# Optimization experiments

Hardware: AMD Instinct MI355X
Metric: run time of the kernel (lower is better)

Reference implementation:

```python
import jax, jax.numpy as jnp
import numpy as np

B, L, H, DH, DM, DFF, V, NL, NP, NT = 4, 2048, 12, 64, 768, 3072, 30522, 12, 2048, 2
LN_EPS = 1e-5       # fast_transformers default LayerNorm eps
EMB_LN_EPS = 1e-12  # BERT embeddings LayerNorm eps
ATT_EPS = 1e-6      # linear attention normalizer eps


def layer_norm(x, w, b, eps):
    m = jnp.mean(x, axis=-1, keepdims=True)
    v = jnp.mean((x - m) ** 2, axis=-1, keepdims=True)
    return (x - m) * jax.lax.rsqrt(v + eps) * w + b


def setup_inputs() -> dict:
    key = jax.random.key(0)
    ks = jax.random.split(key, 24)
    s = 0.02
    d = {
        "input_ids": jax.random.randint(ks[0], (B, L), 0, V),
        "attention_mask": jnp.ones((B, L), jnp.float32),
        "token_type_ids": jnp.zeros((B, L), jnp.int64),
        "word_emb": jax.random.normal(ks[1], (V, DM), jnp.float32) * s,
        "pos_emb": jax.random.normal(ks[2], (NP, DM), jnp.float32) * s,
        "type_emb": jax.random.normal(ks[3], (NT, DM), jnp.float32) * s,
        "emb_ln_w": jnp.ones((DM,), jnp.float32),
        "emb_ln_b": jnp.zeros((DM,), jnp.float32),
        "Wq": jax.random.normal(ks[4], (NL, DM, DM), jnp.float32) * s,
        "bq": jnp.zeros((NL, DM), jnp.float32),
        "Wk": jax.random.normal(ks[5], (NL, DM, DM), jnp.float32) * s,
        "bk": jnp.zeros((NL, DM), jnp.float32),
        "Wv": jax.random.normal(ks[6], (NL, DM, DM), jnp.float32) * s,
        "bv": jnp.zeros((NL, DM), jnp.float32),
        "Wo": jax.random.normal(ks[7], (NL, DM, DM), jnp.float32) * s,
        "bo": jnp.zeros((NL, DM), jnp.float32),
        "ln1_w": jnp.ones((NL, DM), jnp.float32),
        "ln1_b": jnp.zeros((NL, DM), jnp.float32),
        "W1": jax.random.normal(ks[8], (NL, DFF, DM), jnp.float32) * s,
        "b1": jnp.zeros((NL, DFF), jnp.float32),
        "W2": jax.random.normal(ks[9], (NL, DM, DFF), jnp.float32) * s,
        "b2": jnp.zeros((NL, DM), jnp.float32),
        "ln2_w": jnp.ones((NL, DM), jnp.float32),
        "ln2_b": jnp.zeros((NL, DM), jnp.float32),
    }
    return d


def _encoder(x, mask, Wq, bq, Wk, bk, Wv, bv, Wo, bo, ln1_w, ln1_b, W1, b1, W2, b2, ln2_w, ln2_b):
    b, l = x.shape[:2]
    for i in range(NL):
        # linear attention (fast_transformers): phi = elu + 1
        q = (x @ Wq[i].T + bq[i]).reshape(b, l, H, DH)
        k = (x @ Wk[i].T + bk[i]).reshape(b, l, H, DH)
        v = (x @ Wv[i].T + bv[i]).reshape(b, l, H, DH)
        Q = jax.nn.elu(q) + 1.0
        K = (jax.nn.elu(k) + 1.0) * mask[:, :, None, None]  # zero padded keys
        KV = jnp.einsum('nshd,nshm->nhmd', K, v)            # [b,H,DH(m=val),DH(d=key)]
        Z = 1.0 / (jnp.einsum('nlhd,nhd->nlh', Q, K.sum(axis=1)) + ATT_EPS)
        a = jnp.einsum('nlhd,nhmd,nlh->nlhm', Q, KV, Z).reshape(b, l, DM)
        a = a @ Wo[i].T + bo[i]
        x = layer_norm(x + a, ln1_w[i], ln1_b[i], LN_EPS)
        y = jax.nn.gelu(x @ W1[i].T + b1[i], approximate=False)
        y = y @ W2[i].T + b2[i]
        x = layer_norm(x + y, ln2_w[i], ln2_b[i], LN_EPS)
    return x


def reference(input_ids, attention_mask, token_type_ids, word_emb, pos_emb, type_emb,
              emb_ln_w, emb_ln_b, Wq, bq, Wk, bk, Wv, bv, Wo, bo,
              ln1_w, ln1_b, W1, b1, W2, b2, ln2_w, ln2_b):
    b, l = input_ids.shape
    e = word_emb[input_ids] + pos_emb[:l][None, :, :] + type_emb[token_type_ids]
    x = layer_norm(e, emb_ln_w, emb_ln_b, EMB_LN_EPS)
    return _encoder(x, attention_mask, Wq, bq, Wk, bk, Wv, bv, Wo, bo,
                    ln1_w, ln1_b, W1, b1, W2, b2, ln2_w, ln2_b)
```

## Files before the change

### kernel.cpp

```cpp
#include <hip/hip_runtime.h>
#include <math.h>

#define B_   4
#define L_   2048
#define H_   12
#define DH_  64
#define DM_  768
#define DFF_ 3072
#define NL_  12
#define M_   (B_*L_)
#define NCH_ 32
#define QLD_ 2304
#define LN_EPS_  1e-5f
#define EMB_EPS_ 1e-12f
#define ATT_EPS_ 1e-6f

typedef unsigned short u16;
typedef __bf16 bf16x8 __attribute__((ext_vector_type(8)));
typedef float  f32x4  __attribute__((ext_vector_type(4)));

__device__ __forceinline__ u16 f2b(float f) {
  unsigned u = __builtin_bit_cast(unsigned, f);
  u += 0x7fffu + ((u >> 16) & 1u);
  return (u16)(u >> 16);
}
__device__ __forceinline__ float b2f(u16 s) {
  return __builtin_bit_cast(float, (unsigned)((unsigned)s << 16));
}
__device__ __forceinline__ float wredsum(float v) {
  #pragma unroll
  for (int o = 32; o > 0; o >>= 1) v += __shfl_xor(v, o, 64);
  return v;
}
__device__ __forceinline__ void gld16(const void* g, void* l) {
  __builtin_amdgcn_global_load_lds(
      (const __attribute__((address_space(1))) void*)g,
      (__attribute__((address_space(3))) void*)l, 16, 0, 0);
}

__global__ __launch_bounds__(256) void cvt_bf16(const float* __restrict__ in,
                                                u16* __restrict__ out, int n4) {
  int i = blockIdx.x * 256 + threadIdx.x;
  if (i >= n4) return;
  float4 f = ((const float4*)in)[i];
  ushort4 o;
  o.x = f2b(f.x); o.y = f2b(f.y); o.z = f2b(f.z); o.w = f2b(f.w);
  ((ushort4*)out)[i] = o;
}

__global__ __launch_bounds__(256) void cvt_bf16_qkv(const float* __restrict__ in,
                                                    u16* __restrict__ out, int ro) {
  int i = blockIdx.x * 256 + threadIdx.x;
  if (i >= NL_*DM_*DM_/4) return;
  int row = i / 192;
  int c4  = (i % 192) * 4;
  int l = row / DM_, r = row % DM_;
  float4 f = ((const float4*)in)[i];
  ushort4 o;
  o.x = f2b(f.x); o.y = f2b(f.y); o.z = f2b(f.z); o.w = f2b(f.w);
  *(ushort4*)(out + ((size_t)l*QLD_ + ro + r)*DM_ + c4) = o;
}

__global__ __launch_bounds__(256) void fuse_bias(const float* __restrict__ bq,
    const float* __restrict__ bk, const float* __restrict__ bv, float* __restrict__ out) {
  int i = blockIdx.x * 256 + threadIdx.x;
  if (i >= NL_*QLD_) return;
  int l = i / QLD_, r = i % QLD_;
  float v = r < DM_ ? bq[l*DM_ + r] : r < 2*DM_ ? bk[l*DM_ + r - DM_] : bv[l*DM_ + r - 2*DM_];
  out[i] = v;
}

__global__ __launch_bounds__(256) void embed_ln(
    const int* __restrict__ ids, const int* __restrict__ tts,
    const float* __restrict__ we, const float* __restrict__ pe,
    const float* __restrict__ te, const float* __restrict__ lw,
    const float* __restrict__ lb, float* __restrict__ x32, u16* __restrict__ xb)
{
  int row  = blockIdx.x * 4 + (threadIdx.x >> 6);
  int lane = threadIdx.x & 63;
  int l  = row & (L_ - 1);
  int id = ids[row];
  int tt = tts[row];
  const float* wr = we + (size_t)id * DM_;
  const float* pr = pe + (size_t)l  * DM_;
  const float* tr = te + (size_t)tt * DM_;
  float v[12]; float s = 0.f;
  #pragma unroll
  for (int j = 0; j < 12; j++) { int c = j*64 + lane; v[j] = wr[c] + pr[c] + tr[c]; s += v[j]; }
  s = wredsum(s);
  float m = s * (1.f/768.f);
  float q = 0.f;
  #pragma unroll
  for (int j = 0; j < 12; j++) { float d = v[j] - m; q += d*d; }
  q = wredsum(q);
  float rs = rsqrtf(q * (1.f/768.f) + EMB_EPS_);
  float* xo = x32 + (size_t)row * DM_;
  u16*   bo = xb  + (size_t)row * DM_;
  #pragma unroll
  for (int j = 0; j < 12; j++) {
    int c = j*64 + lane;
    float o = (v[j] - m) * rs * lw[c] + lb[c];
    xo[c] = o; bo[c] = f2b(o);
  }
}

__global__ __launch_bounds__(256) void ln_res(
    float* __restrict__ x32, const float* __restrict__ t32,
    const float* __restrict__ lw, const float* __restrict__ lb,
    u16* __restrict__ xb, float eps)
{
  int row  = blockIdx.x * 4 + (threadIdx.x >> 6);
  int lane = threadIdx.x & 63;
  float* xr = x32 + (size_t)row * DM_;
  const float* tr = t32 + (size_t)row * DM_;
  float v[12]; float s = 0.f;
  #pragma unroll
  for (int j = 0; j < 12; j++) { int c = j*64 + lane; v[j] = xr[c] + tr[c]; s += v[j]; }
  s = wredsum(s);
  float m = s * (1.f/768.f);
  float q = 0.f;
  #pragma unroll
  for (int j = 0; j < 12; j++) { float d = v[j] - m; q += d*d; }
  q = wredsum(q);
  float rs = rsqrtf(q * (1.f/768.f) + eps);
  u16* bo = xb + (size_t)row * DM_;
  #pragma unroll
  for (int j = 0; j < 12; j++) {
    int c = j*64 + lane;
    float o = (v[j] - m) * rs * lw[c] + lb[c];
    xr[c] = o; bo[c] = f2b(o);
  }
}

template<int EPI>
__global__ __launch_bounds__(256)
void gemm_gl(const u16* __restrict__ A, const u16* __restrict__ Bw,
             const float* __restrict__ bias,
             u16* __restrict__ Co, float* __restrict__ Cf,
             int M, int N, int K, int ldc)
{
  __shared__ alignas(16) u16 sA[128*32];
  __shared__ alignas(16) u16 sB[128*32];
  const int tid  = threadIdx.x;
  const int lane = tid & 63;
  const int w    = tid >> 6;
  const int wr = w >> 1, wc = w & 1;
  const int row0 = blockIdx.x * 128;
  const int col0 = blockIdx.y * 128;
  const int grow = tid >> 2;
  const int gcol = (tid & 3) * 8;
  const int lr = lane & 15;
  const int lk = (lane >> 4) * 8;

  const u16* Ap = A  + (size_t)(row0 + grow) * K + gcol;
  const u16* Bp = Bw + (size_t)(col0 + grow) * K + gcol;
  u16* sAw0 = sA + w*512;
  u16* sAw1 = sA + 2048 + w*512;
  u16* sBw0 = sB + w*512;
  u16* sBw1 = sB + 2048 + w*512;

  f32x4 acc[4][4];
  #pragma unroll
  for (int i = 0; i < 4; i++)
    #pragma unroll
    for (int j = 0; j < 4; j++) acc[i][j] = (f32x4){0.f,0.f,0.f,0.f};

  for (int kt = 0; kt < K; kt += 32) {
    gld16(Ap + kt,                  sAw0);
    gld16(Ap + kt + (size_t)64*K,   sAw1);
    gld16(Bp + kt,                  sBw0);
    gld16(Bp + kt + (size_t)64*K,   sBw1);
    __syncthreads();
    bf16x8 af[4], bv[4];
    #pragma unroll
    for (int m = 0; m < 4; m++) af[m] = *(const bf16x8*)(sA + (wr*64 + m*16 + lr)*32 + lk);
    #pragma unroll
    for (int n = 0; n < 4; n++) bv[n] = *(const bf16x8*)(sB + (wc*64 + n*16 + lr)*32 + lk);
    #pragma unroll
    for (int m = 0; m < 4; m++)
      #pragma unroll
      for (int n = 0; n < 4; n++)
        acc[m][n] = __builtin_amdgcn_mfma_f32_16x16x32_bf16(af[m], bv[n], acc[m][n], 0, 0, 0);
    __syncthreads();
  }

  #pragma unroll
  for (int m = 0; m < 4; m++) {
    const int row_b = row0 + wr*64 + m*16 + (lane >> 4) * 4;
    #pragma unroll
    for (int n = 0; n < 4; n++) {
      const int col = col0 + wc*64 + n*16 + lr;
      const float bvb = bias[col];
      #pragma unroll
      for (int r = 0; r < 4; r++) {
        float v = acc[m][n][r] + bvb;
        if constexpr (EPI == 4) { if (col < 2*DM_) v = v > 0.f ? v + 1.f : expf(v); }
        if constexpr (EPI == 2) v = 0.5f * v * (1.f + erff(v * 0.70710678118654752f));
        const size_t off = (size_t)(row_b + r) * ldc + col;
        if constexpr (EPI == 3) Cf[off] = v;
        else                    Co[off] = f2b(v);
      }
    }
  }
}

__global__ __launch_bounds__(256)
void gemm_n64(const u16* __restrict__ A, const u16* __restrict__ Bw,
              const float* __restrict__ bias, float* __restrict__ Cf,
              int M, int N, int K, int ldc)
{
  __shared__ alignas(16) u16 sA[128*64];
  __shared__ alignas(16) u16 sB[64*64];
  const int tid  = threadIdx.x;
  const int lane = tid & 63;
  const int w    = tid >> 6;
  const int row0 = blockIdx.x * 128;
  const int col0 = blockIdx.y * 64;
  const int lr = lane & 15;
  const int g  = lane >> 4;
  const int srow = lane >> 3;
  const int acol = (((lane & 7) ^ srow) * 8);

  f32x4 acc[2][4];
  #pragma unroll
  for (int i = 0; i < 2; i++)
    #pragma unroll
    for (int j = 0; j < 4; j++) acc[i][j] = (f32x4){0.f,0.f,0.f,0.f};

  const u16* ApA = A  + (size_t)(row0)*K;
  const u16* BpB = Bw + (size_t)(col0)*K;

  for (int kt = 0; kt < K; kt += 64) {
    #pragma unroll
    for (int j = 0; j < 4; j++)
      gld16(ApA + (size_t)(w*32 + j*8 + srow)*K + kt + acol, sA + (w*32 + j*8)*64);
    #pragma unroll
    for (int j = 0; j < 2; j++)
      gld16(BpB + (size_t)(w*16 + j*8 + srow)*K + kt + acol, sB + (w*16 + j*8)*64);
    __syncthreads();
    #pragma unroll
    for (int kk = 0; kk < 2; kk++) {
      bf16x8 af[2], bv[4];
      #pragma unroll
      for (int m = 0; m < 2; m++) {
        const int R = w*32 + m*16 + lr;
        const int gg = (kk*4 + g) ^ (lr & 7);
        af[m] = *(const bf16x8*)(sA + R*64 + gg*8);
      }
      #pragma unroll
      for (int n = 0; n < 4; n++) {
        const int R = n*16 + lr;
        const int gg = (kk*4 + g) ^ (lr & 7);
        bv[n] = *(const bf16x8*)(sB + R*64 + gg*8);
      }
      #pragma unroll
      for (int m = 0; m < 2; m++)
        #pragma unroll
        for (int n = 0; n < 4; n++)
          acc[m][n] = __builtin_amdgcn_mfma_f32_16x16x32_bf16(af[m], bv[n], acc[m][n], 0, 0, 0);
    }
    __syncthreads();
  }

  #pragma unroll
  for (int m = 0; m < 2; m++) {
    const int row_b = row0 + w*32 + m*16 + (lane >> 4) * 4;
    #pragma unroll
    for (int n = 0; n < 4; n++) {
      const int col = col0 + n*16 + lr;
      const float bvb = bias[col];
      #pragma unroll
      for (int r = 0; r < 4; r++)
        Cf[(size_t)(row_b + r) * ldc + col] = acc[m][n][r] + bvb;
    }
  }
}

__global__ __launch_bounds__(256) void kv_part(
    const u16* __restrict__ qkv, const float* __restrict__ mask,
    float* __restrict__ kvp, float* __restrict__ ksp)
{
  __shared__ float sK[64*64];
  __shared__ float sV[64*64];
  const int bh = blockIdx.x;
  const int b = bh / H_, h = bh % H_;
  const int s0 = blockIdx.y * 64;
  const int t = threadIdx.x;
  const u16* kb = qkv + DM_;
  const u16* vb = qkv + 2*DM_;
  #pragma unroll
  for (int r = 0; r < 2; r++) {
    int idx = r*256 + t;
    int sr = idx >> 3;
    int c  = (idx & 7) * 8;
    int sg = s0 + sr;
    size_t base = ((size_t)(b*L_ + sg)) * QLD_ + h*DH_ + c;
    uint4 kk = *(const uint4*)(kb + base);
    uint4 vv = *(const uint4*)(vb + base);
    float mk = mask[b*L_ + sg];
    const u16* kp = (const u16*)&kk;
    const u16* vp = (const u16*)&vv;
    #pragma unroll
    for (int j = 0; j < 8; j++) {
      sK[sr*64 + c + j] = b2f(kp[j]) * mk;
      sV[sr*64 + c + j] = b2f(vp[j]);
    }
  }
  __syncthreads();
  const int m0 = (t >> 4) * 4;
  const int d0 = (t & 15) * 4;
  float acc[4][4] = {{0.f}};
  float ks[4] = {0.f, 0.f, 0.f, 0.f};
  for (int s = 0; s < 64; s++) {
    float4 vm = *(const float4*)(sV + s*64 + m0);
    float4 kk = *(const float4*)(sK + s*64 + d0);
    float vmv[4] = {vm.x, vm.y, vm.z, vm.w};
    float kkv[4] = {kk.x, kk.y, kk.z, kk.w};
    #pragma unroll
    for (int i = 0; i < 4; i++)
      #pragma unroll
      for (int j = 0; j < 4; j++) acc[i][j] += vmv[i] * kkv[j];
    if (t < 16) { ks[0] += kkv[0]; ks[1] += kkv[1]; ks[2] += kkv[2]; ks[3] += kkv[3]; }
  }
  float* o = kvp + ((size_t)bh*NCH_ + blockIdx.y) * 4096;
  #pragma unroll
  for (int i = 0; i < 4; i++) {
    float4 wv = {acc[i][0], acc[i][1], acc[i][2], acc[i][3]};
    *(float4*)(o + (m0 + i)*64 + d0) = wv;
  }
  if (t < 16) {
    float* ko = ksp + ((size_t)bh*NCH_ + blockIdx.y) * 64;
    #pragma unroll
    for (int j = 0; j < 4; j++) ko[d0 + j] = ks[j];
  }
}

__global__ __launch_bounds__(256) void kv_reduce(
    const float* __restrict__ kvp, const float* __restrict__ ksp,
    float* __restrict__ kv, float* __restrict__ ksum)
{
  const int bh = blockIdx.x;
  const int i = blockIdx.y * 256 + threadIdx.x;
  float s = 0.f;
  #pragma unroll 8
  for (int c = 0; c < NCH_; c++) s += kvp[((size_t)bh*NCH_ + c)*4096 + i];
  kv[(size_t)bh*4096 + i] = s;
  if (blockIdx.y == 0 && threadIdx.x < 64) {
    float q = 0.f;
    #pragma unroll 8
    for (int c = 0; c < NCH_; c++) q += ksp[((size_t)bh*NCH_ + c)*64 + threadIdx.x];
    ksum[bh*64 + threadIdx.x] = q;
  }
}

__global__ __launch_bounds__(256) void attn_av(
    const u16* __restrict__ qkv, const float* __restrict__ kv,
    const float* __restrict__ ksum, u16* __restrict__ ab)
{
  __shared__ alignas(16) u16 sQ[128*72];
  __shared__ alignas(16) u16 sKV[64*72];
  __shared__ float sKs[64];
  __shared__ float sZ[128];
  const int bh = blockIdx.x;
  const int b = bh / H_, h = bh % H_;
  const int l0 = blockIdx.y * 128;
  const int t = threadIdx.x;
  const int lane = t & 63;
  const int w = t >> 6;
  for (int i = t; i < 4096; i += 256)
    sKV[(i >> 6)*72 + (i & 63)] = f2b(kv[(size_t)bh*4096 + i]);
  if (t < 64) sKs[t] = ksum[bh*64 + t];
  #pragma unroll
  for (int r = 0; r < 4; r++) {
    int idx = r*256 + t;
    int s = idx >> 3;
    int c = (idx & 7) * 8;
    *(uint4*)(sQ + s*72 + c) =
        *(const uint4*)(qkv + ((size_t)(b*L_ + l0 + s)) * QLD_ + h*DH_ + c);
  }
  __syncthreads();
  {
    int row = t >> 1, half = t & 1;
    float zd = 0.f;
    #pragma unroll
    for (int ch = 0; ch < 4; ch++) {
      bf16x8 qv = *(const bf16x8*)(sQ + row*72 + half*32 + ch*8);
      #pragma unroll
      for (int j = 0; j < 8; j++) zd += (float)qv[j] * sKs[half*32 + ch*8 + j];
    }
    zd += __shfl_xor(zd, 1, 64);
    if (half == 0) sZ[row] = 1.f / (zd + ATT_EPS_);
  }
  const int lr = lane & 15, lk = (lane >> 4) * 8;
  f32x4 acc[2][4];
  #pragma unroll
  for (int m = 0; m < 2; m++)
    #pragma unroll
    for (int n = 0; n < 4; n++) acc[m][n] = (f32x4){0.f,0.f,0.f,0.f};
  #pragma unroll
  for (int kk = 0; kk < 2; kk++) {
    bf16x8 af[2], bv[4];
    #pragma unroll
    for (int m = 0; m < 2; m++) af[m] = *(const bf16x8*)(sQ + (w*32 + m*16 + lr)*72 + kk*32 + lk);
    #pragma unroll
    for (int n = 0; n < 4; n++) bv[n] = *(const bf16x8*)(sKV + (n*16 + lr)*72 + kk*32 + lk);
    #pragma unroll
    for (int m = 0; m < 2; m++)
      #pragma unroll
      for (int n = 0; n < 4; n++)
        acc[m][n] = __builtin_amdgcn_mfma_f32_16x16x32_bf16(af[m], bv[n], acc[m][n], 0, 0, 0);
  }
  __syncthreads();
  #pragma unroll
  for (int m = 0; m < 2; m++) {
    const int row_l = w*32 + m*16 + (lane >> 4) * 4;
    #pragma unroll
    for (int n = 0; n < 4; n++) {
      const int col = n*16 + lr;
      #pragma unroll
      for (int r = 0; r < 4; r++) {
        float v = acc[m][n][r] * sZ[row_l + r];
        ab[((size_t)(b*L_ + l0 + row_l + r)) * DM_ + h*DH_ + col] = f2b(v);
      }
    }
  }
}

__global__ __launch_bounds__(256) void copyf4(const float4* __restrict__ in,
                                              float4* __restrict__ out, int n4) {
  int i = blockIdx.x * 256 + threadIdx.x;
  if (i < n4) out[i] = in[i];
}

extern "C" void kernel_launch(void* const* d_in, const int* in_sizes, int n_in,
                              void* d_out, int out_size, void* d_ws, size_t ws_size,
                              hipStream_t stream)
{
  const int*   ids  = (const int*)d_in[0];
  const float* mask = (const float*)d_in[1];
  const int*   tts  = (const int*)d_in[2];
  const float* we   = (const float*)d_in[3];
  const float* pe   = (const float*)d_in[4];
  const float* te   = (const float*)d_in[5];
  const float* elw  = (const float*)d_in[6];
  const float* elb  = (const float*)d_in[7];
  const float* Wq   = (const float*)d_in[8];
  const float* bq   = (const float*)d_in[9];
  const float* Wk   = (const float*)d_in[10];
  const float* bk   = (const float*)d_in[11];
  const float* Wv   = (const float*)d_in[12];
  const float* bv   = (const float*)d_in[13];
  const float* Wo   = (const float*)d_in[14];
  const float* bo   = (const float*)d_in[15];
  const float* l1w  = (const float*)d_in[16];
  const float* l1b  = (const float*)d_in[17];
  const float* W1   = (const float*)d_in[18];
  const float* b1   = (const float*)d_in[19];
  const float* W2   = (const float*)d_in[20];
  const float* b2   = (const float*)d_in[21];
  const float* l2w  = (const float*)d_in[22];
  const float* l2b  = (const float*)d_in[23];

  char* p = (char*)d_ws;
  auto alloc = [&](size_t n) -> char* {
    char* r = p; p += (n + 255) & ~(size_t)255; return r;
  };
  const size_t SQ = (size_t)NL_ * DM_ * DM_;
  const size_t SF = (size_t)NL_ * DFF_ * DM_;
  u16*  wqkvb = (u16*)alloc((size_t)NL_ * QLD_ * DM_ * 2);
  u16*  wob   = (u16*)alloc(SQ * 2);
  u16*  w1b   = (u16*)alloc(SF * 2);
  u16*  w2b   = (u16*)alloc(SF * 2);
  float* bqkv = (float*)alloc((size_t)NL_ * QLD_ * 4);
  float* x32  = (float*)alloc((size_t)M_ * DM_ * 4);
  float* t32  = (float*)alloc((size_t)M_ * DM_ * 4);
  u16*  xb    = (u16*)alloc((size_t)M_ * DM_ * 2);
  u16*  qkv   = (u16*)alloc((size_t)M_ * QLD_ * 2);
  u16*  abuf  = (u16*)alloc((size_t)M_ * DM_ * 2);
  u16*  ybuf  = (u16*)alloc((size_t)M_ * DFF_ * 2);
  float* kvb  = (float*)alloc((size_t)(B_*H_*DH_*DH_ + B_*H_*DH_) * 4);
  float* ksm  = kvb + (size_t)B_*H_*DH_*DH_;
  float* ksp  = (float*)alloc((size_t)B_*H_*NCH_*DH_ * 4);
  float* kvp  = t32;

  const int nq4 = (int)(SQ/4);
  cvt_bf16_qkv<<<(nq4+255)/256, 256, 0, stream>>>(Wq, wqkvb, 0);
  cvt_bf16_qkv<<<(nq4+255)/256, 256, 0, stream>>>(Wk, wqkvb, DM_);
  cvt_bf16_qkv<<<(nq4+255)/256, 256, 0, stream>>>(Wv, wqkvb, 2*DM_);
  cvt_bf16<<<nq4/256, 256, 0, stream>>>(Wo, wob, nq4);
  cvt_bf16<<<(int)(SF/4/256), 256, 0, stream>>>(W1, w1b, (int)(SF/4));
  cvt_bf16<<<(int)(SF/4/256), 256, 0, stream>>>(W2, w2b, (int)(SF/4));
  fuse_bias<<<(NL_*QLD_+255)/256, 256, 0, stream>>>(bq, bk, bv, bqkv);

  embed_ln<<<M_/4, 256, 0, stream>>>(ids, tts, we, pe, te, elw, elb, x32, xb);

  for (int il = 0; il < NL_; ++il) {
    const u16* wqkv = wqkvb + (size_t)il * QLD_ * DM_;
    const u16* wo = wob + (size_t)il * DM_ * DM_;
    const u16* w1 = w1b + (size_t)il * DFF_ * DM_;
    const u16* w2 = w2b + (size_t)il * DFF_ * DM_;

    gemm_gl<4><<<dim3(M_/128, QLD_/128), 256, 0, stream>>>(
        xb, wqkv, bqkv + (size_t)il*QLD_, qkv, nullptr, M_, QLD_, DM_, QLD_);

    kv_part<<<dim3(B_*H_, NCH_), 256, 0, stream>>>(qkv, mask, kvp, ksp);
    kv_reduce<<<dim3(B_*H_, 16), 256, 0, stream>>>(kvp, ksp, kvb, ksm);
    attn_av<<<dim3(B_*H_, L_/128), 256, 0, stream>>>(qkv, kvb, ksm, abuf);

    gemm_n64<<<dim3(M_/128, DM_/64), 256, 0, stream>>>(
        abuf, wo, bo + (size_t)il*DM_, t32, M_, DM_, DM_, DM_);
    ln_res<<<M_/4, 256, 0, stream>>>(x32, t32, l1w + (size_t)il*DM_, l1b + (size_t)il*DM_, xb, LN_EPS_);

    gemm_gl<2><<<dim3(M_/128, DFF_/128), 256, 0, stream>>>(
        xb, w1, b1 + (size_t)il*DFF_, ybuf, nullptr, M_, DFF_, DM_, DFF_);
    gemm_n64<<<dim3(M_/128, DM_/64), 256, 0, stream>>>(
        ybuf, w2, b2 + (size_t)il*DM_, t32, M_, DM_, DFF_, DM_);
    ln_res<<<M_/4, 256, 0, stream>>>(x32, t32, l2w + (size_t)il*DM_, l2b + (size_t)il*DM_, xb, LN_EPS_);
  }

  copyf4<<<(M_*DM_/4)/256, 256, 0, stream>>>((const float4*)x32, (float4*)d_out, M_*DM_/4);
}
```

Before: 3.401 ms.

## Double GEMM K-tile to 64 with XOR-swizzled LDS layout

The bf16 MFMA GEMM now loads a 64-wide K slice per iteration instead of 32, which halves the number of barrier pairs per K loop. Global-to-LDS loads use an XOR swizzle of the 16-byte column chunk by row so that fragment reads from LDS avoid bank conflicts, and the reads apply the matching swizzle. LDS use doubles to 32 KB per block, which may lower occupancy. There is still no double-buffering.

```diff
diff --git a/kernel.cpp b/kernel.cpp
--- a/kernel.cpp
+++ b/kernel.cpp
@@ -139,25 +139,18 @@
              u16* __restrict__ Co, float* __restrict__ Cf,
              int M, int N, int K, int ldc)
 {
-  __shared__ alignas(16) u16 sA[128*32];
-  __shared__ alignas(16) u16 sB[128*32];
+  __shared__ alignas(16) u16 sA[128*64];
+  __shared__ alignas(16) u16 sB[128*64];
   const int tid  = threadIdx.x;
   const int lane = tid & 63;
   const int w    = tid >> 6;
   const int wr = w >> 1, wc = w & 1;
   const int row0 = blockIdx.x * 128;
   const int col0 = blockIdx.y * 128;
-  const int grow = tid >> 2;
-  const int gcol = (tid & 3) * 8;
   const int lr = lane & 15;
-  const int lk = (lane >> 4) * 8;
-
-  const u16* Ap = A  + (size_t)(row0 + grow) * K + gcol;
-  const u16* Bp = Bw + (size_t)(col0 + grow) * K + gcol;
-  u16* sAw0 = sA + w*512;
-  u16* sAw1 = sA + 2048 + w*512;
-  u16* sBw0 = sB + w*512;
-  u16* sBw1 = sB + 2048 + w*512;
+  const int g  = lane >> 4;
+  const int srow = lane >> 3;
+  const int acol = (((lane & 7) ^ srow) * 8);
 
   f32x4 acc[4][4];
   #pragma unroll
@@ -165,22 +158,30 @@
     #pragma unroll
     for (int j = 0; j < 4; j++) acc[i][j] = (f32x4){0.f,0.f,0.f,0.f};
 
-  for (int kt = 0; kt < K; kt += 32) {
-    gld16(Ap + kt,                  sAw0);
-    gld16(Ap + kt + (size_t)64*K,   sAw1);
-    gld16(Bp + kt,                  sBw0);
-    gld16(Bp + kt + (size_t)64*K,   sBw1);
+  const u16* Ap = A  + (size_t)row0 * K;
+  const u16* Bp = Bw + (size_t)col0 * K;
+
+  for (int kt = 0; kt < K; kt += 64) {
+    #pragma unroll
+    for (int j = 0; j < 4; j++) {
+      gld16(Ap + (size_t)(w*32 + j*8 + srow)*K + kt + acol, sA + (w*32 + j*8)*64);
+      gld16(Bp + (size_t)(w*32 + j*8 + srow)*K + kt + acol, sB + (w*32 + j*8)*64);
+    }
     __syncthreads();
-    bf16x8 af[4], bv[4];
-    #pragma unroll
-    for (int m = 0; m < 4; m++) af[m] = *(const bf16x8*)(sA + (wr*64 + m*16 + lr)*32 + lk);
-    #pragma unroll
-    for (int n = 0; n < 4; n++) bv[n] = *(const bf16x8*)(sB + (wc*64 + n*16 + lr)*32 + lk);
-    #pragma unroll
-    for (int m = 0; m < 4; m++)
-      #pragma unroll
-      for (int n = 0; n < 4; n++)
-        acc[m][n] = __builtin_amdgcn_mfma_f32_16x16x32_bf16(af[m], bv[n], acc[m][n], 0, 0, 0);
+    #pragma unroll
+    for (int kk = 0; kk < 2; kk++) {
+      const int gg = ((kk*4 + g) ^ (lr & 7)) * 8;
+      bf16x8 af[4], bv[4];
+      #pragma unroll
+      for (int m = 0; m < 4; m++) af[m] = *(const bf16x8*)(sA + (wr*64 + m*16 + lr)*64 + gg);
+      #pragma unroll
+      for (int n = 0; n < 4; n++) bv[n] = *(const bf16x8*)(sB + (wc*64 + n*16 + lr)*64 + gg);
+      #pragma unroll
+      for (int m = 0; m < 4; m++)
+        #pragma unroll
+        for (int n = 0; n < 4; n++)
+          acc[m][n] = __builtin_amdgcn_mfma_f32_16x16x32_bf16(af[m], bv[n], acc[m][n], 0, 0, 0);
+    }
     __syncthreads();
   }
 
```

New measurement: 3.227 ms. 5.1% less time.
